# Kernel optimization log

Measured on AMD Instinct MI355X. Metric: run time of the kernel, lower is better.

## Reference

```python
import jax, jax.numpy as jnp
import numpy as np

B, T, D = 2, 2048, 768
H, DH = 12, 64  # heads, head_dim; H*DH == D


def setup_inputs() -> dict:
    key = jax.random.key(0)
    ks = jax.random.split(key, 9)
    s = 0.02  # small init scale like GPT-2
    return {
        "x": jax.random.normal(ks[0], (B, T, D), dtype=jnp.float32),
        "Wq": jax.random.normal(ks[1], (D, H * DH), dtype=jnp.float32) * s,
        "bq": jax.random.normal(ks[2], (H * DH,), dtype=jnp.float32) * s,
        "Wk": jax.random.normal(ks[3], (D, H * DH), dtype=jnp.float32) * s,
        "bk": jax.random.normal(ks[4], (H * DH,), dtype=jnp.float32) * s,
        "Wv": jax.random.normal(ks[5], (D, H * DH), dtype=jnp.float32) * s,
        "bv": jax.random.normal(ks[6], (H * DH,), dtype=jnp.float32) * s,
        "Wo": jax.random.normal(ks[7], (H * DH, H * DH), dtype=jnp.float32) * s,
        "bo": jax.random.normal(ks[8], (H * DH,), dtype=jnp.float32) * s,
    }


def reference(x, Wq, bq, Wk, bk, Wv, bv, Wo, bo):
    b, t, _ = x.shape
    # projections -> [b, t, H, DH] -> [b, H, t, DH]
    q = (x @ Wq + bq).reshape(b, t, H, DH).transpose(0, 2, 1, 3)
    k = (x @ Wk + bk).reshape(b, t, H, DH).transpose(0, 2, 1, 3)
    v = (x @ Wv + bv).reshape(b, t, H, DH).transpose(0, 2, 1, 3)
    # full O(T^2) score matrix, matching the naive torch module
    scores = jnp.einsum("bhqd,bhkd->bhqk", q, k)
    causal = jnp.tril(jnp.ones((t, t), dtype=bool))  # True = keep
    scores = jnp.where(causal, scores, -jnp.inf)
    weights = jax.nn.softmax(scores / jnp.sqrt(jnp.float32(DH)), axis=-1)
    # dropout with p=0.0 is identity
    ctx = jnp.einsum("bhqk,bhkd->bhqd", weights, v)
    ctx = ctx.transpose(0, 2, 1, 3).reshape(b, t, H * DH)
    return ctx @ Wo + bo
```

## Files before the change

kernel.cpp:

```cpp
#include <hip/hip_runtime.h>
#include <hip/hip_bf16.h>
#include <math.h>

typedef unsigned short u16;
typedef unsigned int u32;
typedef __attribute__((ext_vector_type(8))) short short8v;
typedef __attribute__((ext_vector_type(4))) float f32x4;
typedef __attribute__((ext_vector_type(16))) float f32x16;

#define BB 2
#define TT 2048
#define DD 768
#define HH 12
#define DHH 64
#define MM 4096
#define NSLOT 36
#define QSC 0.18033688f

#define SWZ(r, kb) (((r) * 128) + ((kb) ^ (((r) & 7) << 4)))

typedef __attribute__((address_space(1))) void gas_void;
typedef __attribute__((address_space(3))) void las_void;
#define GLL(g, l) __builtin_amdgcn_global_load_lds((gas_void*)(g), (las_void*)(l), 16, 0, 0)

__device__ const unsigned char SLOT_QT[36] = {
    7,7,7,7,7,7,7, 6,6,6,6,6,6, 5,5,5,5,5, 4,4,4,4, 3,3,3, 2,2, 1,
    7,6,5,4,3,2,1,0};
__device__ const unsigned char SLOT_C[36] = {
    0,1,2,3,4,5,6, 0,1,2,3,4,5, 0,1,2,3,4, 0,1,2,3, 0,1,2, 0,1, 0,
    7,6,5,4,3,2,1,0};
__device__ const unsigned char BASEF[8] = {0, 27, 25, 22, 18, 13, 7, 0};

__device__ __forceinline__ u16 f2bf(float f) {
    union { float f; unsigned u; } v; v.f = f;
    unsigned r = v.u + 0x7fff + ((v.u >> 16) & 1);
    return (u16)(r >> 16);
}
__device__ __forceinline__ u32 pkpair(float a, float b) {
    union { __hip_bfloat162 h; u32 u; } v;
    v.h = __float22bfloat162_rn(make_float2(a, b));
    return v.u;
}
__device__ __forceinline__ float fexp2(float x) {
#if __has_builtin(__builtin_amdgcn_exp2f)
    return __builtin_amdgcn_exp2f(x);
#else
    return exp2f(x);
#endif
}
__device__ __forceinline__ float bfhi(u32 p) {
    union { u32 u; float f; } v; v.u = p & 0xffff0000u; return v.f;
}
__device__ __forceinline__ float bflo(u32 p) {
    union { u32 u; float f; } v; v.u = p << 16; return v.f;
}

__global__ __launch_bounds__(256) void prep(
    const float* __restrict__ x, u16* __restrict__ xb,
    const float* __restrict__ W0, const float* __restrict__ W1,
    const float* __restrict__ W2, const float* __restrict__ W3,
    u16* __restrict__ T0, u16* __restrict__ T1,
    u16* __restrict__ T2, u16* __restrict__ T3)
{
    __shared__ float tile[64][65];
    const int bid = blockIdx.x;
    const int t = threadIdx.x;

    if (bid < 3072) {
        const int i = bid * 256 + t;
        const float4 v = ((const float4*)x)[i];
        union { u16 s[4]; uint2 u; } o;
        o.s[0] = f2bf(v.x); o.s[1] = f2bf(v.y); o.s[2] = f2bf(v.z); o.s[3] = f2bf(v.w);
        ((uint2*)xb)[i] = o.u;
        return;
    }

    const int idx = bid - 3072;
    const int z = idx / 144;
    const int r2 = idx - z * 144;
    const int k0 = (r2 / 12) * 64, n0 = (r2 % 12) * 64;
    const float* __restrict__ W = (z == 0) ? W0 : (z == 1) ? W1 : (z == 2) ? W2 : W3;
    u16* __restrict__ T = (z == 0) ? T0 : (z == 1) ? T1 : (z == 2) ? T2 : T3;

    const int rr = t >> 4, c4 = (t & 15) * 4;
    #pragma unroll
    for (int j = 0; j < 4; ++j) {
        const int r = rr + j * 16;
        const float4 v = *(const float4*)&W[(size_t)(k0 + r) * DD + n0 + c4];
        tile[r][c4 + 0] = v.x; tile[r][c4 + 1] = v.y;
        tile[r][c4 + 2] = v.z; tile[r][c4 + 3] = v.w;
    }
    __syncthreads();
    #pragma unroll
    for (int j = 0; j < 4; ++j) {
        const int r = rr + j * 16;
        union { u16 s[4]; uint2 u; } o;
        #pragma unroll
        for (int jj = 0; jj < 4; ++jj) o.s[jj] = f2bf(tile[c4 + jj][r]);
        *(uint2*)&T[(size_t)(n0 + r) * DD + k0 + c4] = o.u;
    }
}

__global__ __launch_bounds__(256) void gemm_bt(
    const u16* __restrict__ A,
    const u16* __restrict__ Bt0, const u16* __restrict__ Bt1, const u16* __restrict__ Bt2,
    const float* __restrict__ b0, const float* __restrict__ b1, const float* __restrict__ b2,
    u16* __restrict__ oQ, u16* __restrict__ oK, u16* __restrict__ oVt)
{
    const int lin = blockIdx.x;
    const int cpx = gridDim.x >> 3;
    const int swz = (lin & 7) * cpx + (lin >> 3);
    const int mt  = swz / 18;
    const int r18 = swz - mt * 18;
    const int mode = r18 / 6;
    const int m0 = mt * 128, n0 = (r18 - mode * 6) * 128;

    const u16* __restrict__ Bt = (mode == 1) ? Bt1 : (mode == 2) ? Bt2 : Bt0;
    const float* __restrict__ bias = (mode == 1) ? b1 : (mode == 2) ? b2 : b0;

    __shared__ __attribute__((aligned(16))) unsigned char AsB[2][16384];
    __shared__ __attribute__((aligned(16))) unsigned char BsB[2][16384];

    const int tid = threadIdx.x, lane = tid & 63, w = tid >> 6;
    const int wr = w >> 1, wc = w & 1;
    const int lr = lane >> 4, lc = lane & 15;
    const int srcoff = 16 * ((lane & 7) ^ (lane >> 3));

#define GSTAGE(k0_, bufi) do {                                                 \
        _Pragma("unroll")                                                      \
        for (int i_ = 0; i_ < 4; ++i_) {                                       \
            const int r_ = w * 32 + i_ * 8 + (lane >> 3);                      \
            GLL((const char*)A  + ((size_t)(m0 + r_) * DD + (k0_)) * 2 + srcoff,\
                (char*)AsB[bufi] + w * 4096 + i_ * 1024);                      \
            GLL((const char*)Bt + ((size_t)(n0 + r_) * DD + (k0_)) * 2 + srcoff,\
                (char*)BsB[bufi] + w * 4096 + i_ * 1024);                      \
        }                                                                      \
    } while (0)

    f32x4 acc[4][4];
    #pragma unroll
    for (int m = 0; m < 4; ++m)
        #pragma unroll
        for (int n = 0; n < 4; ++n) acc[m][n] = (f32x4){0.f, 0.f, 0.f, 0.f};

    GSTAGE(0, 0);
    __syncthreads();

    int cur = 0;
    #pragma unroll 1
    for (int k0 = 0; k0 < DD; k0 += 64) {
        if (k0 + 64 < DD) GSTAGE(k0 + 64, cur ^ 1);

        #pragma unroll
        for (int s = 0; s < 2; ++s) {
            short8v af[4], bf[4];
            #pragma unroll
            for (int m = 0; m < 4; ++m)
                af[m] = *(const short8v*)((const char*)AsB[cur] +
                         SWZ(wr * 64 + m * 16 + lc, s * 64 + lr * 16));
            #pragma unroll
            for (int n = 0; n < 4; ++n)
                bf[n] = *(const short8v*)((const char*)BsB[cur] +
                         SWZ(wc * 64 + n * 16 + lc, s * 64 + lr * 16));
            #pragma unroll
            for (int m = 0; m < 4; ++m)
                #pragma unroll
                for (int n = 0; n < 4; ++n)
                    acc[m][n] = __builtin_amdgcn_mfma_f32_16x16x32_bf16(
                        af[m], bf[n], acc[m][n], 0, 0, 0);
        }

        __syncthreads();
        cur ^= 1;
    }
#undef GSTAGE

    #pragma unroll
    for (int n = 0; n < 4; ++n) {
        const int ng = n0 + wc * 64 + n * 16 + lc;
        const float bv = bias[ng];
        #pragma unroll
        for (int m = 0; m < 4; ++m) {
            const int mg0 = m0 + wr * 64 + m * 16 + lr * 4;
            if (mode == 2) {
                const int bb = mg0 >> 11, tp = mg0 & 2047;
                const int h = ng >> 6, d = ng & 63;
                const size_t idx = (size_t)(bb * HH + h) * (TT * DHH)
                                 + (tp >> 6) * 4096 + ((tp >> 3) & 7) * 512
                                 + d * 8 + (tp & 7);
                union { u16 s[4]; uint2 u; } o;
                #pragma unroll
                for (int r = 0; r < 4; ++r) o.s[r] = f2bf(acc[m][n][r] + bv);
                *(uint2*)&oVt[idx] = o.u;
            } else if (mode == 1) {
                const int h = ng >> 6, d = ng & 63;
                #pragma unroll
                for (int r = 0; r < 4; ++r) {
                    const int mg = mg0 + r;
                    const int bb = mg >> 11, tp = mg & 2047;
                    oK[(size_t)(bb * HH + h) * (TT * DHH)
                       + (tp >> 6) * 4096 + (d >> 3) * 512 + (tp & 63) * 8 + (d & 7)] =
                        f2bf(acc[m][n][r] + bv);
                }
            } else {
                const int h = ng >> 6, d = ng & 63;
                #pragma unroll
                for (int r = 0; r < 4; ++r) {
                    const int mg = mg0 + r;
                    const int bb = mg >> 11, tp = mg & 2047;
                    oQ[((size_t)(bb * HH + h) * TT + tp) * DHH + d] =
                        f2bf((acc[m][n][r] + bv) * QSC);
                }
            }
        }
    }
}

__global__ __launch_bounds__(256) void gemm_out64(
    const u16* __restrict__ A, const u16* __restrict__ Bt,
    const float* __restrict__ bias, float* __restrict__ oF)
{
    const int lin = blockIdx.x;
    const int cpx = gridDim.x >> 3;
    const int swz = (lin & 7) * cpx + (lin >> 3);
    const int m0 = (swz / 6) * 64;
    const int n0 = (swz % 6) * 128;

    __shared__ __attribute__((aligned(16))) unsigned char AsB[2][8192];
    __shared__ __attribute__((aligned(16))) unsigned char BsB[2][16384];

    const int tid = threadIdx.x, lane = tid & 63, w = tid >> 6;
    const int wr = w >> 1, wc = w & 1;
    const int lr = lane >> 4, lc = lane & 15;
    const int srcoff = 16 * ((lane & 7) ^ (lane >> 3));

#define GSTAGE(k0_, bufi) do {                                                 \
        _Pragma("unroll")                                                      \
        for (int i_ = 0; i_ < 2; ++i_) {                                       \
            const int ra_ = w * 16 + i_ * 8 + (lane >> 3);                     \
            GLL((const char*)A  + ((size_t)(m0 + ra_) * DD + (k0_)) * 2 + srcoff,\
                (char*)AsB[bufi] + w * 2048 + i_ * 1024);                      \
        }                                                                      \
        _Pragma("unroll")                                                      \
        for (int i_ = 0; i_ < 4; ++i_) {                                       \
            const int rb_ = w * 32 + i_ * 8 + (lane >> 3);                     \
            GLL((const char*)Bt + ((size_t)(n0 + rb_) * DD + (k0_)) * 2 + srcoff,\
                (char*)BsB[bufi] + w * 4096 + i_ * 1024);                      \
        }                                                                      \
    } while (0)

    f32x4 acc[2][4];
    #pragma unroll
    for (int m = 0; m < 2; ++m)
        #pragma unroll
        for (int n = 0; n < 4; ++n) acc[m][n] = (f32x4){0.f, 0.f, 0.f, 0.f};

    GSTAGE(0, 0);
    __syncthreads();

    int cur = 0;
    #pragma unroll 1
    for (int k0 = 0; k0 < DD; k0 += 64) {
        if (k0 + 64 < DD) GSTAGE(k0 + 64, cur ^ 1);

        #pragma unroll
        for (int s = 0; s < 2; ++s) {
            short8v af[2], bf[4];
            #pragma unroll
            for (int m = 0; m < 2; ++m)
                af[m] = *(const short8v*)((const char*)AsB[cur] +
                         SWZ(wr * 32 + m * 16 + lc, s * 64 + lr * 16));
            #pragma unroll
            for (int n = 0; n < 4; ++n)
                bf[n] = *(const short8v*)((const char*)BsB[cur] +
                         SWZ(wc * 64 + n * 16 + lc, s * 64 + lr * 16));
            #pragma unroll
            for (int m = 0; m < 2; ++m)
                #pragma unroll
                for (int n = 0; n < 4; ++n)
                    acc[m][n] = __builtin_amdgcn_mfma_f32_16x16x32_bf16(
                        af[m], bf[n], acc[m][n], 0, 0, 0);
        }

        __syncthreads();
        cur ^= 1;
    }
#undef GSTAGE

    #pragma unroll
    for (int n = 0; n < 4; ++n) {
        const int ng = n0 + wc * 64 + n * 16 + lc;
        const float bv = bias[ng];
        #pragma unroll
        for (int m = 0; m < 2; ++m) {
            const int mg0 = m0 + wr * 32 + m * 16 + lr * 4;
            #pragma unroll
            for (int r = 0; r < 4; ++r)
                oF[(size_t)(mg0 + r) * DD + ng] = acc[m][n][r] + bv;
        }
    }
}

__global__ __launch_bounds__(512) void attn_fwd(
    const u16* __restrict__ qb, const u16* __restrict__ kbf,
    const u16* __restrict__ vtb, u16* __restrict__ partO,
    float* __restrict__ partL)
{
    __shared__ __attribute__((aligned(16))) unsigned char smem[65536];

    const int bid = blockIdx.x;
    const int sp = bid / 24;
    const int bh = bid - sp * 24;
    const int qt = SLOT_QT[sp], c = SLOT_C[sp];
    const int kts = c * 4;

    const int tid = threadIdx.x, lane = tid & 63, w = tid >> 6;
    const int l31 = lane & 31, hi = lane >> 5;

    {
        const char* kbase = (const char*)kbf + (size_t)bh * (TT * DHH * 2)
                          + (size_t)kts * 8192;
        const char* vbase = (const char*)vtb + (size_t)bh * (TT * DHH * 2)
                          + (size_t)kts * 8192;
        const int off = w * 1024;
        #pragma unroll
        for (int t = 0; t < 4; ++t) {
            GLL(kbase + t * 8192 + off + lane * 16,
                (char*)smem + t * 8192 + off);
            GLL(vbase + t * 8192 + off + lane * 16,
                (char*)smem + 32768 + t * 8192 + off);
        }
    }

    short8v aq[4];
    {
        const u16* qrow = qb + ((size_t)bh * TT + qt * 256 + w * 32 + l31) * DHH;
        #pragma unroll
        for (int s4 = 0; s4 < 4; ++s4)
            aq[s4] = *(const short8v*)(qrow + s4 * 16 + hi * 8);
    }

    f32x16 accO[2];
    #pragma unroll
    for (int i = 0; i < 16; ++i) { accO[0][i] = 0.f; accO[1][i] = 0.f; }
    float lreg = 0.f;

    __syncthreads();

    const int qmin = qt * 256 + w * 32;
    #pragma unroll
    for (int t = 0; t < 4; ++t) {
        const int kt = kts + t;
        if (kt * 64 <= qmin + 31) {
            const unsigned char* Kb = smem + t * 8192;
            const unsigned char* Vb = smem + 32768 + t * 8192;

            f32x16 st[2];
            #pragma unroll
            for (int i = 0; i < 16; ++i) { st[0][i] = 0.f; st[1][i] = 0.f; }
            __builtin_amdgcn_s_setprio(1);
            #pragma unroll
            for (int s4 = 0; s4 < 4; ++s4) {
                #pragma unroll
                for (int kf = 0; kf < 2; ++kf) {
                    const short8v ak = *(const short8v*)(Kb +
                        (s4 * 2 + hi) * 1024 + (kf * 32 + l31) * 16);
                    st[kf] = __builtin_amdgcn_mfma_f32_32x32x16_bf16(ak, aq[s4], st[kf], 0, 0, 0);
                }
            }
            __builtin_amdgcn_s_setprio(0);

            if (kt * 64 + 63 > qmin) {
                const int rowrel = qmin + l31 - kt * 64;
                #pragma unroll
                for (int kf = 0; kf < 2; ++kf)
                    #pragma unroll
                    for (int reg = 0; reg < 16; ++reg) {
                        const int kloc = kf * 32 + (reg & 3) + 8 * (reg >> 2) + 4 * hi;
                        if (kloc > rowrel) st[kf][reg] = -3.0e38f;
                    }
            }

            float rs4[4] = {0.f, 0.f, 0.f, 0.f};
            #pragma unroll
            for (int kf = 0; kf < 2; ++kf)
                #pragma unroll
                for (int reg = 0; reg < 16; ++reg) {
                    const float p = fexp2(st[kf][reg]);
                    st[kf][reg] = p;
                    rs4[reg & 3] += p;
                }
            float rs = (rs4[0] + rs4[1]) + (rs4[2] + rs4[3]);
            {
                u32 a, b;
                union { float f; u32 u; } cv; cv.f = rs;
                a = cv.u; b = cv.u;
                asm volatile("v_permlane32_swap_b32 %0, %1" : "+v"(a), "+v"(b));
                union { u32 u; float f; } pa, pb; pa.u = a; pb.u = b;
                const float partner = hi ? pa.f : pb.f;
                rs += partner;
            }
            lreg += rs;

            __builtin_amdgcn_s_setprio(1);
            #pragma unroll
            for (int ka = 0; ka < 4; ++ka) {
                const int kf = ka >> 1;
                const int rb0 = 4 * ((ka & 1) * 2);
                const int rb1 = 4 * ((ka & 1) * 2 + 1);
                u32 P0 = pkpair(st[kf][rb0 + 0], st[kf][rb0 + 1]);
                u32 P1 = pkpair(st[kf][rb0 + 2], st[kf][rb0 + 3]);
                u32 Q0 = pkpair(st[kf][rb1 + 0], st[kf][rb1 + 1]);
                u32 Q1 = pkpair(st[kf][rb1 + 2], st[kf][rb1 + 3]);
                asm volatile("v_permlane32_swap_b32 %0, %1" : "+v"(P0), "+v"(Q0));
                asm volatile("v_permlane32_swap_b32 %0, %1" : "+v"(P1), "+v"(Q1));
                union { u32 wd[4]; short8v v; } u;
                u.wd[0] = P0; u.wd[1] = P1; u.wd[2] = Q0; u.wd[3] = Q1;
                #pragma unroll
                for (int dc = 0; dc < 2; ++dc) {
                    const short8v bv = *(const short8v*)(Vb +
                        (ka * 2 + hi) * 1024 + (dc * 32 + l31) * 16);
                    accO[dc] = __builtin_amdgcn_mfma_f32_32x32x16_bf16(u.v, bv, accO[dc], 0, 0, 0);
                }
            }
            __builtin_amdgcn_s_setprio(0);
        }
    }

    const int gslot = bh * NSLOT + sp;
    if (hi == 0)
        partL[(size_t)gslot * 256 + w * 32 + l31] = lreg;
    u16* po = partO + (size_t)gslot * 16384;
    #pragma unroll
    for (int reg = 0; reg < 16; ++reg) {
        const int qrow = (reg & 3) + 8 * (reg >> 2) + 4 * hi;
        #pragma unroll
        for (int dc = 0; dc < 2; ++dc)
            po[(w * 32 + qrow) * 64 + dc * 32 + l31] = f2bf(accO[dc][reg]);
    }
}

__global__ __launch_bounds__(256) void attn_combine(
    const u16* __restrict__ partO, const float* __restrict__ partL,
    u16* __restrict__ ctx)
{
    const int bid = blockIdx.x;
    const int q64 = bid / 24, bh = bid - q64 * 24;
    const int b = bh / HH, h = bh - b * HH;
    const int qt = q64 >> 2;
    const int sub = q64 & 3;
    const int tid = threadIdx.x, q = tid >> 2, dg = tid & 3;
    const int prow = sub * 64 + q;

    float lsum = 0.f;
    float acc[16];
    #pragma unroll
    for (int j = 0; j < 16; ++j) acc[j] = 0.f;

#define ACCUM(gs) do {                                                         \
        lsum += partL[(size_t)(gs) * 256 + prow];                              \
        const u16* po_ = partO + (size_t)(gs) * 16384 + prow * 64 + dg * 16;   \
        _Pragma("unroll")                                                      \
        for (int v_ = 0; v_ < 2; ++v_) {                                       \
            const uint4 pk = *(const uint4*)(po_ + v_ * 8);                    \
            acc[v_*8+0] += bflo(pk.x); acc[v_*8+1] += bfhi(pk.x);              \
            acc[v_*8+2] += bflo(pk.y); acc[v_*8+3] += bfhi(pk.y);              \
            acc[v_*8+4] += bflo(pk.z); acc[v_*8+5] += bfhi(pk.z);              \
            acc[v_*8+6] += bflo(pk.w); acc[v_*8+7] += bfhi(pk.w);              \
        }                                                                      \
    } while (0)

    const int basef = bh * NSLOT + BASEF[qt];
    #pragma unroll 1
    for (int cc = 0; cc < qt; ++cc) ACCUM(basef + cc);
    ACCUM(bh * NSLOT + (35 - qt));
#undef ACCUM

    const float inv = 1.f / lsum;
    u16* dst = ctx + (size_t)(b * TT + qt * 256 + prow) * DD + h * 64 + dg * 16;
    #pragma unroll
    for (int v = 0; v < 2; ++v) {
        uint4 o;
        o.x = pkpair(acc[v*8+0] * inv, acc[v*8+1] * inv);
        o.y = pkpair(acc[v*8+2] * inv, acc[v*8+3] * inv);
        o.z = pkpair(acc[v*8+4] * inv, acc[v*8+5] * inv);
        o.w = pkpair(acc[v*8+6] * inv, acc[v*8+7] * inv);
        *(uint4*)(dst + v * 8) = o;
    }
}

extern "C" void kernel_launch(void* const* d_in, const int* in_sizes, int n_in,
                              void* d_out, int out_size, void* d_ws, size_t ws_size,
                              hipStream_t stream) {
    (void)in_sizes; (void)n_in; (void)out_size; (void)ws_size;
    const float* x  = (const float*)d_in[0];
    const float* Wq = (const float*)d_in[1];
    const float* bq = (const float*)d_in[2];
    const float* Wk = (const float*)d_in[3];
    const float* bk = (const float*)d_in[4];
    const float* Wv = (const float*)d_in[5];
    const float* bv = (const float*)d_in[6];
    const float* Wo = (const float*)d_in[7];
    const float* bo = (const float*)d_in[8];
    float* out = (float*)d_out;

    u16* xb    = (u16*)d_ws;
    u16* WtQ   = xb + (size_t)MM * DD;
    u16* WtK   = WtQ + (size_t)DD * DD;
    u16* WtV   = WtK + (size_t)DD * DD;
    u16* WtO   = WtV + (size_t)DD * DD;
    u16* qbuf  = WtO + (size_t)DD * DD;
    u16* kbuf  = qbuf + (size_t)MM * DD;
    u16* vtbuf = kbuf + (size_t)MM * DD;
    u16* ctxb  = vtbuf + (size_t)MM * DD;
    u16* pO    = ctxb + (size_t)MM * DD;
    float* pL  = (float*)(pO + (size_t)24 * NSLOT * 16384);

    prep<<<dim3(3648), 256, 0, stream>>>(x, xb, Wq, Wk, Wv, Wo, WtQ, WtK, WtV, WtO);
    gemm_bt<<<dim3(576), 256, 0, stream>>>(xb, WtQ, WtK, WtV, bq, bk, bv,
                                           qbuf, kbuf, vtbuf);
    attn_fwd<<<dim3(24 * NSLOT), 512, 0, stream>>>(qbuf, kbuf, vtbuf, pO, pL);
    attn_combine<<<dim3(768), 256, 0, stream>>>(pO, pL, ctxb);
    gemm_out64<<<dim3(384), 256, 0, stream>>>(ctxb, WtO, bo, out);
}
```

Baseline: 86.98 us.

## Fuse split-KV combine into attention kernel via last-block atomic tickets

Removes the separate attn_combine launch. Each attention block now bumps an atomic ticket for its (head, query-tile) after writing its partial output, and the last block to arrive reduces all partials and writes the normalized context. This saves a kernel launch and the gap between kernels, at the cost of threadfences, an atomic, a memset launch, and a serialized reduction tail executed by 512 threads per tile with a heavier per-thread load.

```diff
diff --git a/kernel.cpp b/kernel.cpp
--- a/kernel.cpp
+++ b/kernel.cpp
@@ -304,9 +304,11 @@
 __global__ __launch_bounds__(512) void attn_fwd(
     const u16* __restrict__ qb, const u16* __restrict__ kbf,
     const u16* __restrict__ vtb, u16* __restrict__ partO,
-    float* __restrict__ partL)
+    float* __restrict__ partL, u16* __restrict__ ctx,
+    int* __restrict__ tickets)
 {
     __shared__ __attribute__((aligned(16))) unsigned char smem[65536];
+    __shared__ int lastflag;
 
     const int bid = blockIdx.x;
     const int sp = bid / 24;
@@ -438,30 +440,31 @@
         for (int dc = 0; dc < 2; ++dc)
             po[(w * 32 + qrow) * 64 + dc * 32 + l31] = f2bf(accO[dc][reg]);
     }
-}
-
-__global__ __launch_bounds__(256) void attn_combine(
-    const u16* __restrict__ partO, const float* __restrict__ partL,
-    u16* __restrict__ ctx)
-{
-    const int bid = blockIdx.x;
-    const int q64 = bid / 24, bh = bid - q64 * 24;
-    const int b = bh / HH, h = bh - b * HH;
-    const int qt = q64 >> 2;
-    const int sub = q64 & 3;
-    const int tid = threadIdx.x, q = tid >> 2, dg = tid & 3;
-    const int prow = sub * 64 + q;
-
-    float lsum = 0.f;
-    float acc[16];
-    #pragma unroll
-    for (int j = 0; j < 16; ++j) acc[j] = 0.f;
+
+    __threadfence();
+    __syncthreads();
+    if (tid == 0) {
+        const int old = atomicAdd(&tickets[bh * 8 + qt], 1);
+        lastflag = (old == qt);
+    }
+    __syncthreads();
+    if (!lastflag) return;
+
+    __threadfence();
+    {
+        const int b2 = bh / HH, h2 = bh - b2 * HH;
+        const int q = tid >> 1, half = tid & 1;
+
+        float lsum = 0.f;
+        float acc[32];
+        #pragma unroll
+        for (int j = 0; j < 32; ++j) acc[j] = 0.f;
 
 #define ACCUM(gs) do {                                                         \
-        lsum += partL[(size_t)(gs) * 256 + prow];                              \
-        const u16* po_ = partO + (size_t)(gs) * 16384 + prow * 64 + dg * 16;   \
+        lsum += partL[(size_t)(gs) * 256 + q];                                 \
+        const u16* po_ = partO + (size_t)(gs) * 16384 + q * 64 + half * 32;    \
         _Pragma("unroll")                                                      \
-        for (int v_ = 0; v_ < 2; ++v_) {                                       \
+        for (int v_ = 0; v_ < 4; ++v_) {                                       \
             const uint4 pk = *(const uint4*)(po_ + v_ * 8);                    \
             acc[v_*8+0] += bflo(pk.x); acc[v_*8+1] += bfhi(pk.x);              \
             acc[v_*8+2] += bflo(pk.y); acc[v_*8+3] += bfhi(pk.y);              \
@@ -470,22 +473,23 @@
         }                                                                      \
     } while (0)
 
-    const int basef = bh * NSLOT + BASEF[qt];
-    #pragma unroll 1
-    for (int cc = 0; cc < qt; ++cc) ACCUM(basef + cc);
-    ACCUM(bh * NSLOT + (35 - qt));
+        const int basef = bh * NSLOT + BASEF[qt];
+        #pragma unroll 1
+        for (int cc = 0; cc < qt; ++cc) ACCUM(basef + cc);
+        ACCUM(bh * NSLOT + (35 - qt));
 #undef ACCUM
 
-    const float inv = 1.f / lsum;
-    u16* dst = ctx + (size_t)(b * TT + qt * 256 + prow) * DD + h * 64 + dg * 16;
-    #pragma unroll
-    for (int v = 0; v < 2; ++v) {
-        uint4 o;
-        o.x = pkpair(acc[v*8+0] * inv, acc[v*8+1] * inv);
-        o.y = pkpair(acc[v*8+2] * inv, acc[v*8+3] * inv);
-        o.z = pkpair(acc[v*8+4] * inv, acc[v*8+5] * inv);
-        o.w = pkpair(acc[v*8+6] * inv, acc[v*8+7] * inv);
-        *(uint4*)(dst + v * 8) = o;
+        const float inv = 1.f / lsum;
+        u16* dst = ctx + (size_t)(b2 * TT + qt * 256 + q) * DD + h2 * 64 + half * 32;
+        #pragma unroll
+        for (int v = 0; v < 4; ++v) {
+            uint4 o;
+            o.x = pkpair(acc[v*8+0] * inv, acc[v*8+1] * inv);
+            o.y = pkpair(acc[v*8+2] * inv, acc[v*8+3] * inv);
+            o.z = pkpair(acc[v*8+4] * inv, acc[v*8+5] * inv);
+            o.w = pkpair(acc[v*8+6] * inv, acc[v*8+7] * inv);
+            *(uint4*)(dst + v * 8) = o;
+        }
     }
 }
 
@@ -515,11 +519,13 @@
     u16* ctxb  = vtbuf + (size_t)MM * DD;
     u16* pO    = ctxb + (size_t)MM * DD;
     float* pL  = (float*)(pO + (size_t)24 * NSLOT * 16384);
-
+    int* tickets = (int*)(pL + (size_t)24 * NSLOT * 256);
+
+    hipMemsetAsync(tickets, 0, 24 * 8 * sizeof(int), stream);
     prep<<<dim3(3648), 256, 0, stream>>>(x, xb, Wq, Wk, Wv, Wo, WtQ, WtK, WtV, WtO);
     gemm_bt<<<dim3(576), 256, 0, stream>>>(xb, WtQ, WtK, WtV, bq, bk, bv,
                                            qbuf, kbuf, vtbuf);
-    attn_fwd<<<dim3(24 * NSLOT), 512, 0, stream>>>(qbuf, kbuf, vtbuf, pO, pL);
-    attn_combine<<<dim3(768), 256, 0, stream>>>(pO, pL, ctxb);
+    attn_fwd<<<dim3(24 * NSLOT), 512, 0, stream>>>(qbuf, kbuf, vtbuf, pO, pL,
+                                                   ctxb, tickets);
     gemm_out64<<<dim3(384), 256, 0, stream>>>(ctxb, WtO, bo, out);
 }
```

Measured after the change: 329.6 us. 279% more time.
